# Optimization experiments

Measured on AMD Instinct MI355X. Metric: run time of the kernel, lower is better.

## Reference

```python
import jax, jax.numpy as jnp
from jax import lax
import numpy as np

DN = ('NHWC', 'HWIO', 'NHWC')  # NHWC activations, HWIO kernels (TF layout)
EPS = 1e-3


def setup_inputs() -> dict:
    key = jax.random.key(0)
    ks = jax.random.split(key, 6)
    B, H, W, C = 16, 64, 64, 256
    x = jax.random.normal(ks[0], (B, H, W, C), jnp.float32)
    # per-sample predicted kernels (scaled to keep activations well-conditioned)
    depthwise_kernels = jax.random.normal(ks[1], (B, 3, 3, C, C), jnp.float32) * 0.02
    pointwise_kernels = jax.random.normal(ks[2], (B, 1, 1, C, C), jnp.float32) * 0.06
    biases = jax.random.normal(ks[3], (B, C), jnp.float32) * 0.1
    # shared trailing Conv2D layer params
    conv_w = jax.random.normal(ks[4], (3, 3, C, C), jnp.float32) * 0.02
    conv_b = jnp.zeros((C,), jnp.float32)
    return dict(x=x, depthwise_kernels=depthwise_kernels,
                pointwise_kernels=pointwise_kernels, biases=biases,
                conv_w=conv_w, conv_b=conv_b)


def _instance_norm(x):
    # tf.nn.moments over spatial dims (population variance), eps=0.001
    mean = jnp.mean(x, axis=(1, 2), keepdims=True)
    var = jnp.var(x, axis=(1, 2), keepdims=True)
    return (x - mean) * lax.rsqrt(var + EPS)


def _reflect_pad_hw(x, p=1):
    pad = [(0, 0)] * (x.ndim - 3) + [(p, p), (p, p), (0, 0)]
    return jnp.pad(x, pad, mode='reflect')


def _per_sample_conv(xi, dk, pk, bi):
    # xi: [H,W,C]; dk: [3,3,C,Cm]; pk: [1,1,Cm,Co]; bi: [Co]
    xp = _reflect_pad_hw(xi)[None]  # [1,H+2,W+2,C]
    y = lax.conv_general_dilated(xp, dk, (1, 1), 'VALID', dimension_numbers=DN)
    y = lax.conv_general_dilated(y, pk, (1, 1), 'VALID', dimension_numbers=DN)
    return (y + bi)[0]


def reference(x, depthwise_kernels, pointwise_kernels, biases, conv_w, conv_b):
    x = _instance_norm(x)
    # per-sample kernels -> vmap over batch (replaces tf.map_fn)
    x = jax.vmap(_per_sample_conv)(x, depthwise_kernels, pointwise_kernels, biases)
    # shared Conv2D: reflect pad + VALID conv + bias
    xp = _reflect_pad_hw(x)
    y = lax.conv_general_dilated(xp, conv_w, (1, 1), 'VALID', dimension_numbers=DN)
    return y + conv_b
```

## Files before the change

kernel.cpp:

```cpp
#include <hip/hip_runtime.h>


typedef __bf16 bf16x8 __attribute__((ext_vector_type(8)));
typedef float f32x4 __attribute__((ext_vector_type(4)));

__device__ __forceinline__ float bf2f(unsigned short v) {
    return __uint_as_float(((unsigned int)v) << 16);
}
__device__ __forceinline__ unsigned short f2bf(float f) {
    unsigned int u = __float_as_uint(f);
    unsigned int r = (u + 0x7FFFu + ((u >> 16) & 1u)) >> 16;
    return (unsigned short)r;
}
__device__ __forceinline__ float ldg_elem(const void* p, size_t idx, bool isbf) {
    return isbf ? bf2f(((const unsigned short*)p)[idx]) : ((const float*)p)[idx];
}

__device__ __forceinline__ void gload16(const void* g, void* l) {
    __builtin_amdgcn_global_load_lds(
        (__attribute__((address_space(1))) void*)(unsigned long long)g,
        (__attribute__((address_space(3))) void*)(unsigned long long)l,
        16, 0, 0);
}

#define RAW_BARRIER() do { asm volatile("" ::: "memory"); \
                           __builtin_amdgcn_s_barrier();   \
                           asm volatile("" ::: "memory"); } while (0)

__global__ void detect_dtype(const unsigned short* __restrict__ x, int* __restrict__ flag) {
    __shared__ int wild;
    if (threadIdx.x == 0) wild = 0;
    __syncthreads();
    int cnt = 0;
    for (int i = 0; i < 16; ++i) {
        float a = fabsf(bf2f(x[threadIdx.x * 16 + i]));
        if (!(a < 64.f) || (a != 0.f && a < 1e-5f)) cnt++;
    }
    atomicAdd(&wild, cnt);
    __syncthreads();
    if (threadIdx.x == 0) *flag = (wild > 512) ? 0 : 1;
}

__global__ void norm_partial2(const void* __restrict__ x, const int* __restrict__ flag,
                              float* __restrict__ partS, float* __restrict__ partQ) {
    const bool isbf = (*flag != 0);
    const int b = blockIdx.x, ch = blockIdx.y;
    const int t = threadIdx.x;
    const int l = t & 63;
    const int c4 = l * 4;
    const int sp0 = t >> 6;
    const size_t base = ((size_t)(b * 4096 + ch * 128 + sp0)) * 256 + c4;
    float s[4] = {0.f, 0.f, 0.f, 0.f}, q[4] = {0.f, 0.f, 0.f, 0.f};
    if (isbf) {
        for (int i = 0; i < 32; ++i) {
            const unsigned short* p = (const unsigned short*)x + base + (size_t)i * 1024;
            ushort4 v = *(const ushort4*)p;
            float a[4] = {bf2f(v.x), bf2f(v.y), bf2f(v.z), bf2f(v.w)};
#pragma unroll
            for (int j = 0; j < 4; ++j) { s[j] += a[j]; q[j] += a[j] * a[j]; }
        }
    } else {
        for (int i = 0; i < 32; ++i) {
            float4 v = *(const float4*)((const float*)x + base + (size_t)i * 1024);
            float a[4] = {v.x, v.y, v.z, v.w};
#pragma unroll
            for (int j = 0; j < 4; ++j) { s[j] += a[j]; q[j] += a[j] * a[j]; }
        }
    }
    __shared__ float red[4][64][9];
#pragma unroll
    for (int j = 0; j < 4; ++j) { red[sp0][l][j] = s[j]; red[sp0][l][4 + j] = q[j]; }
    __syncthreads();
    if (t < 64) {
#pragma unroll
        for (int j = 0; j < 4; ++j) {
            float ss = red[0][t][j] + red[1][t][j] + red[2][t][j] + red[3][t][j];
            float qq = red[0][t][4 + j] + red[1][t][4 + j] + red[2][t][4 + j] + red[3][t][4 + j];
            int c = t * 4 + j;
            partS[(b * 32 + ch) * 256 + c] = ss;
            partQ[(b * 32 + ch) * 256 + c] = qq;
        }
    }
}

__global__ void norm_finalize2(const float* __restrict__ partS, const float* __restrict__ partQ,
                               float* __restrict__ mean, float* __restrict__ rstd) {
    const int b = blockIdx.x, c = threadIdx.x;
    float s = 0.f, q = 0.f;
    for (int k = 0; k < 32; ++k) {
        s += partS[(b * 32 + k) * 256 + c];
        q += partQ[(b * 32 + k) * 256 + c];
    }
    float m = s * (1.f / 4096.f);
    float v = q * (1.f / 4096.f) - m * m;
    mean[b * 256 + c] = m;
    rstd[b * 256 + c] = rsqrtf(v + 1e-3f);
}

__global__ void norm_apply(const void* __restrict__ x, const int* __restrict__ flag,
                           const float* __restrict__ mean, const float* __restrict__ rstd,
                           unsigned short* __restrict__ xn) {
    const bool isbf = (*flag != 0);
    size_t e = ((size_t)blockIdx.x * 256 + threadIdx.x) * 8;
    int c0 = (int)(e & 255);
    int bc = (int)(e >> 20) * 256 + c0;
    float v[8];
    if (isbf) {
        uint4 raw = *(const uint4*)((const unsigned short*)x + e);
        unsigned int rr[4] = {raw.x, raw.y, raw.z, raw.w};
#pragma unroll
        for (int i = 0; i < 4; ++i) {
            v[2 * i]     = bf2f((unsigned short)(rr[i] & 0xFFFF));
            v[2 * i + 1] = bf2f((unsigned short)(rr[i] >> 16));
        }
    } else {
        float4 f0 = *(const float4*)((const float*)x + e);
        float4 f1 = *(const float4*)((const float*)x + e + 4);
        v[0] = f0.x; v[1] = f0.y; v[2] = f0.z; v[3] = f0.w;
        v[4] = f1.x; v[5] = f1.y; v[6] = f1.z; v[7] = f1.w;
    }
    unsigned int o[4];
#pragma unroll
    for (int i = 0; i < 4; ++i) {
        unsigned short lo = f2bf((v[2 * i]     - mean[bc + 2 * i])     * rstd[bc + 2 * i]);
        unsigned short hi = f2bf((v[2 * i + 1] - mean[bc + 2 * i + 1]) * rstd[bc + 2 * i + 1]);
        o[i] = (unsigned int)lo | ((unsigned int)hi << 16);
    }
    uint4 out; out.x = o[0]; out.y = o[1]; out.z = o[2]; out.w = o[3];
    *(uint4*)(xn + e) = out;
}

template <bool SCALE>
__global__ void transpose_wk(const void* __restrict__ src, const int* __restrict__ flag,
                             unsigned short* __restrict__ dst,
                             int s_per, long dstBStride, int coStride,
                             const float* __restrict__ rstd) {
    __shared__ unsigned short tile[64][66];
    const bool isbf = (*flag != 0);
    const int sl = blockIdx.x;
    const int b = sl / s_per;
    const size_t dbase = (size_t)b * (size_t)dstBStride + (size_t)(sl % s_per) * 256;
    const int ci0 = blockIdx.y * 64, co0 = blockIdx.z * 64;
    const int t = threadIdx.x;
    const int co4 = (t & 15) * 4;
    const int r0 = t >> 4;
#pragma unroll
    for (int i = 0; i < 4; ++i) {
        int r = r0 + i * 16;
        size_t sidx = (size_t)sl * 65536 + (size_t)(ci0 + r) * 256 + co0 + co4;
        if (isbf) {
            ushort4 v = *(const ushort4*)((const unsigned short*)src + sidx);
            tile[r][co4] = v.x; tile[r][co4 + 1] = v.y;
            tile[r][co4 + 2] = v.z; tile[r][co4 + 3] = v.w;
        } else {
            float4 v = *(const float4*)((const float*)src + sidx);
            tile[r][co4] = f2bf(v.x); tile[r][co4 + 1] = f2bf(v.y);
            tile[r][co4 + 2] = f2bf(v.z); tile[r][co4 + 3] = f2bf(v.w);
        }
    }
    __syncthreads();
    const int cip = (t & 31) * 2;
    const int cob = t >> 5;
    float s0 = 1.f, s1 = 1.f;
    if (SCALE) { s0 = rstd[b * 256 + ci0 + cip]; s1 = rstd[b * 256 + ci0 + cip + 1]; }
#pragma unroll
    for (int i = 0; i < 8; ++i) {
        int co = cob + i * 8;
        unsigned short lo = tile[cip][co], hi = tile[cip + 1][co];
        if (SCALE) { lo = f2bf(bf2f(lo) * s0); hi = f2bf(bf2f(hi) * s1); }
        *(unsigned int*)(dst + dbase + (size_t)(co0 + co) * coStride + ci0 + cip) =
            (unsigned int)lo | ((unsigned int)hi << 16);
    }
}

__global__ void corr_kernel(const unsigned short* __restrict__ dkT,
                            const float* __restrict__ mean,
                            float* __restrict__ negcorr) {
    const int b = blockIdx.x;
    const int lane = threadIdx.x & 63;
    const int co = blockIdx.y * 4 + (threadIdx.x >> 6);
    const unsigned short* wp = dkT + (size_t)(b * 256 + co) * 2304;
    const float* mb = mean + b * 256;
    const int ci0 = (lane & 31) * 8;
    float4 ma = *(const float4*)(mb + ci0);
    float4 mc = *(const float4*)(mb + ci0 + 4);
    float mm[8] = {ma.x, ma.y, ma.z, ma.w, mc.x, mc.y, mc.z, mc.w};
    float sum = 0.f;
#pragma unroll
    for (int c = 0; c < 5; ++c) {
        int k = c * 512 + lane * 8;
        if (k < 2304) {
            uint4 w = *(const uint4*)(wp + k);
            unsigned int wsv[4] = {w.x, w.y, w.z, w.w};
#pragma unroll
            for (int j = 0; j < 4; ++j) {
                sum += bf2f((unsigned short)(wsv[j] & 0xFFFF)) * mm[2 * j];
                sum += bf2f((unsigned short)(wsv[j] >> 16)) * mm[2 * j + 1];
            }
        }
    }
#pragma unroll
    for (int off = 32; off > 0; off >>= 1) sum += __shfl_down(sum, off);
    if (lane == 0) negcorr[b * 256 + co] = -sum;
}

template <bool PER_SAMPLE_W, int BIAS_MODE, bool OUT_F32>
__global__ __launch_bounds__(512, 2) void conv3x3_256(const unsigned short* __restrict__ src,
                                                      const int* __restrict__ flag,
                                                      const unsigned short* __restrict__ wT,
                                                      const void* __restrict__ bias,
                                                      void* __restrict__ dst) {
    constexpr int KTOT = 2304;
    extern __shared__ unsigned short smem[];

    const int t = threadIdx.x;
    const int lane = t & 63;
    const int wave = t >> 6;
    const int wr = wave >> 1;
    const int wc = wave & 1;
    const int bid = blockIdx.x + 16 * blockIdx.z;
    const int b  = (bid & 7) + ((bid >> 3) & 1) * 8;
    const int mt = bid >> 4;
    const int m0 = mt * 256;
    const int R0 = mt * 4;
    const unsigned short* srcB = src + (size_t)b * (4096 * 256);
    const unsigned short* wB = wT + (PER_SAMPLE_W ? (size_t)b * 256 * KTOT : (size_t)0);
    const bool in_bf = (BIAS_MODE >= 2) ? (*flag != 0) : true;

    const int wx = t >> 3;
    const int wg = ((t & 7) ^ (wx & 7)) << 3;
    int wrow[6];
#pragma unroll
    for (int u = 0; u < 6; ++u) {
        int r = R0 - 1 + u;
        wrow[u] = (r < 0) ? 1 : (r > 63 ? 62 : r);
    }
    const unsigned short* winsrc[6];
#pragma unroll
    for (int u = 0; u < 6; ++u)
        winsrc[u] = srcB + ((size_t)wrow[u] * 64 + wx) * 256 + wg;
    const unsigned short* bsrc = wB + (size_t)wx * KTOT + wg;

    auto issueB = [&](int jn) {
        const int sn = jn % 9, cgn = jn / 9;
        const int koff = sn * 256 + cgn * 64;
        unsigned short* bdst = smem + 49152 + (jn & 1) * 16384 + wave * 512;
#pragma unroll
        for (int u = 0; u < 4; ++u)
            gload16(bsrc + (size_t)u * 64 * KTOT + koff, bdst + u * 4096);
    };

    f32x4 acc[4][8];
#pragma unroll
    for (int i = 0; i < 4; ++i)
#pragma unroll
        for (int j = 0; j < 8; ++j) acc[i][j] = (f32x4){0.f, 0.f, 0.f, 0.f};

    const int fr = lane & 15;
    const int quad = lane >> 4;
    const int fsw = fr & 7;
    const int ksb0 = (quad ^ fsw) << 3;
    const int ksb1 = ((quad + 4) ^ fsw) << 3;
    const int cn = wc * 128;

#pragma unroll
    for (int u = 0; u < 6; ++u)
        gload16(winsrc[u], smem + u * 4096 + wave * 512);
    issueB(0);

    bf16x8 afp[4][2], bfr[4][2];

    for (int cg = 0; cg < 4; ++cg) {
        const unsigned short* winb = smem + (cg & 1) * 24576;
        for (int s = 0; s < 9; ++s) {
            const int j = cg * 9 + s;
            const int dh = s / 3 - 1;
            const int dw = s % 3 - 1;

            const int keep = (cg < 3) ? ((s == 6 || s == 7) ? 2 : (s == 8 ? 1 : 0)) : 0;
            if (keep == 2)      asm volatile("s_waitcnt vmcnt(2)" ::: "memory");
            else if (keep == 1) asm volatile("s_waitcnt vmcnt(1)" ::: "memory");
            else                asm volatile("s_waitcnt vmcnt(0)" ::: "memory");
            RAW_BARRIER();

            if (j < 35) issueB(j + 1);
            if (cg < 3) {
                unsigned short* wdst = smem + ((cg + 1) & 1) * 24576 + wave * 512;
                const int cgo = (cg + 1) * 64;
                if (s == 5) {
                    gload16(winsrc[0] + cgo, wdst);
                    gload16(winsrc[1] + cgo, wdst + 4096);
                } else if (s == 6) {
                    gload16(winsrc[2] + cgo, wdst + 2 * 4096);
                    gload16(winsrc[3] + cgo, wdst + 3 * 4096);
                } else if (s == 7) {
                    gload16(winsrc[4] + cgo, wdst + 4 * 4096);
                } else if (s == 8) {
                    gload16(winsrc[5] + cgo, wdst + 5 * 4096);
                }
            }

            const unsigned short* Bb = smem + 49152 + (j & 1) * 16384;

#pragma unroll
            for (int n = 0; n < 4; ++n) {
                const unsigned short* rp = Bb + (cn + n * 16 + fr) * 64;
                bfr[n][0] = *(const bf16x8*)(rp + ksb0);
                bfr[n][1] = *(const bf16x8*)(rp + ksb1);
            }
            if (s == 0) {
                const unsigned short* A1 = winb + (wr + 1 + dh) * 4096;
#pragma unroll
                for (int mi = 0; mi < 4; ++mi) {
                    int ww = mi * 16 + fr + dw;
                    ww = (ww < 0) ? 1 : (ww > 63 ? 62 : ww);
                    const int x7 = ww & 7;
                    afp[mi][0] = *(const bf16x8*)(A1 + ww * 64 + ((quad ^ x7) << 3));
                    afp[mi][1] = *(const bf16x8*)(A1 + ww * 64 + (((quad + 4) ^ x7) << 3));
                }
            }

            __builtin_amdgcn_s_setprio(1);
#pragma unroll
            for (int mi = 0; mi < 4; ++mi)
#pragma unroll
                for (int n = 0; n < 4; ++n) {
                    acc[mi][n] = __builtin_amdgcn_mfma_f32_16x16x32_bf16(afp[mi][0], bfr[n][0], acc[mi][n], 0, 0, 0);
                    acc[mi][n] = __builtin_amdgcn_mfma_f32_16x16x32_bf16(afp[mi][1], bfr[n][1], acc[mi][n], 0, 0, 0);
                }
            __builtin_amdgcn_s_setprio(0);

#pragma unroll
            for (int n = 0; n < 4; ++n) {
                const unsigned short* rp = Bb + (cn + (n + 4) * 16 + fr) * 64;
                bfr[n][0] = *(const bf16x8*)(rp + ksb0);
                bfr[n][1] = *(const bf16x8*)(rp + ksb1);
            }

            __builtin_amdgcn_s_setprio(1);
#pragma unroll
            for (int mi = 0; mi < 4; ++mi)
#pragma unroll
                for (int n = 0; n < 4; ++n) {
                    acc[mi][n + 4] = __builtin_amdgcn_mfma_f32_16x16x32_bf16(afp[mi][0], bfr[n][0], acc[mi][n + 4], 0, 0, 0);
                    acc[mi][n + 4] = __builtin_amdgcn_mfma_f32_16x16x32_bf16(afp[mi][1], bfr[n][1], acc[mi][n + 4], 0, 0, 0);
                }
            __builtin_amdgcn_s_setprio(0);

            if (s < 8) {
                const int s1 = s + 1;
                const int dh1 = s1 / 3 - 1;
                const int dw1 = s1 % 3 - 1;
                const unsigned short* A1n = winb + (wr + 1 + dh1) * 4096;
#pragma unroll
                for (int mi = 0; mi < 4; ++mi) {
                    int ww = mi * 16 + fr + dw1;
                    ww = (ww < 0) ? 1 : (ww > 63 ? 62 : ww);
                    const int x7 = ww & 7;
                    afp[mi][0] = *(const bf16x8*)(A1n + ww * 64 + ((quad ^ x7) << 3));
                    afp[mi][1] = *(const bf16x8*)(A1n + ww * 64 + (((quad + 4) ^ x7) << 3));
                }
            }
        }
    }

    const int rbase = quad * 4;
    float bv[8];
#pragma unroll
    for (int n = 0; n < 8; ++n) {
        int nn = cn + n * 16 + fr;
        if (BIAS_MODE == 2)      bv[n] = ldg_elem(bias, b * 256 + nn, in_bf);
        else if (BIAS_MODE == 3) bv[n] = ldg_elem(bias, nn, in_bf);
        else                     bv[n] = 0.f;
    }
#pragma unroll
    for (int m = 0; m < 4; ++m) {
#pragma unroll
        for (int rr = 0; rr < 4; ++rr) {
            int mm = m0 + wr * 64 + m * 16 + rbase + rr;
            size_t rowoff = ((size_t)b * 4096 + mm) * 256;
#pragma unroll
            for (int n = 0; n < 8; ++n) {
                int nn = cn + n * 16 + fr;
                float val = acc[m][n][rr] + bv[n];
                if (OUT_F32) ((float*)dst)[rowoff + nn] = val;
                else         ((unsigned short*)dst)[rowoff + nn] = f2bf(val);
            }
        }
    }
}

template <int KSLICES, bool PER_SAMPLE_W, int BIAS_MODE, bool IS3X3, bool OUT_F32>
__global__ __launch_bounds__(512, 2) void gemm_conv_256(const unsigned short* __restrict__ src,
                                                        const int* __restrict__ flag,
                                                        const unsigned short* __restrict__ wT,
                                                        const void* __restrict__ bias,
                                                        void* __restrict__ dst) {
    constexpr int KTOT = KSLICES * 256;
    constexpr int NKT = KTOT / 64;
    static_assert(NKT >= 2, "pipeline needs >=2 K-tiles");
    extern __shared__ unsigned short smem[];

    const int t = threadIdx.x;
    const int lane = t & 63;
    const int wave = t >> 6;
    const int wr = wave >> 2;
    const int wc = wave & 3;
    const int bid = blockIdx.x + 16 * blockIdx.z;
    const int b  = (bid & 7) + ((bid >> 3) & 1) * 8;
    const int m0 = (bid >> 4) * 256;
    const unsigned short* srcB = src + (size_t)b * (4096 * 256);
    const unsigned short* wB = wT + (PER_SAMPLE_W ? (size_t)b * 256 * KTOT : (size_t)0);
    const bool in_bf = (BIAS_MODE >= 2) ? (*flag != 0) : true;

    const int trow = t >> 3;
    const int tswz = ((t & 7) ^ (trow & 7)) << 3;
    int hU[4], wU[4];
#pragma unroll
    for (int u = 0; u < 4; ++u) {
        int m = m0 + u * 64 + trow;
        hU[u] = m >> 6; wU[u] = m & 63;
    }
    const unsigned short* gBu[4];
#pragma unroll
    for (int u = 0; u < 4; ++u)
        gBu[u] = wB + (size_t)(u * 64 + trow) * KTOT + tswz;

    f32x4 acc[8][4];
#pragma unroll
    for (int i = 0; i < 8; ++i)
#pragma unroll
        for (int j = 0; j < 4; ++j) acc[i][j] = (f32x4){0.f, 0.f, 0.f, 0.f};

    const int fr = lane & 15;
    const int quad = lane >> 4;
    const int fsw = fr & 7;
    const int ks0 = ((quad) ^ fsw) << 3;
    const int ks1 = ((quad + 4) ^ fsw) << 3;
    const int rm = wr * 128;
    const int cn = wc * 64;

#pragma unroll
    for (int kt = 0; kt < 2; ++kt) {
        const int pdh = IS3X3 ? -1 : 0;
        const int pdw = IS3X3 ? -1 : 0;
        const int pchb = (kt & 3) << 6;
        unsigned short* ldsAW = smem + kt * 32768 + wave * 512;
#pragma unroll
        for (int u = 0; u < 4; ++u) {
            int hh = hU[u] + pdh; hh = (hh < 0) ? 1 : (hh > 63 ? 62 : hh);
            int ww = wU[u] + pdw; ww = (ww < 0) ? 1 : (ww > 63 ? 62 : ww);
            gload16(srcB + (size_t)((hh << 6) + ww) * 256 + pchb + tswz, ldsAW + u * 4096);
        }
#pragma unroll
        for (int u = 0; u < 4; ++u)
            gload16(gBu[u] + (size_t)kt * 64, ldsAW + 16384 + u * 4096);
    }
    asm volatile("s_waitcnt vmcnt(8)" ::: "memory");
    RAW_BARRIER();

    bf16x8 af[4][2], bfr[4][2];
    size_t aoff[4];
    int cur_s = -1;

    for (int i = 0; i < NKT; ++i) {
        const int buf = i & 1;
        const unsigned short* As_b = smem + buf * 32768;
        const unsigned short* Bs_b = As_b + 16384;
        unsigned short* ldsAW = smem + buf * 32768 + wave * 512;
        const int kt2 = i + 2;
        const bool st = (kt2 < NKT);

#pragma unroll
        for (int m = 0; m < 4; ++m) {
            const unsigned short* rp = As_b + (rm + m * 16 + fr) * 64;
            af[m][0] = *(const bf16x8*)(rp + ks0);
            af[m][1] = *(const bf16x8*)(rp + ks1);
        }
#pragma unroll
        for (int n = 0; n < 2; ++n) {
            const unsigned short* rp = Bs_b + (cn + n * 16 + fr) * 64;
            bfr[n][0] = *(const bf16x8*)(rp + ks0);
            bfr[n][1] = *(const bf16x8*)(rp + ks1);
        }
        __builtin_amdgcn_s_setprio(1);
#pragma unroll
        for (int m = 0; m < 4; ++m)
#pragma unroll
            for (int n = 0; n < 2; ++n) {
                acc[m][n] = __builtin_amdgcn_mfma_f32_16x16x32_bf16(af[m][0], bfr[n][0], acc[m][n], 0, 0, 0);
                acc[m][n] = __builtin_amdgcn_mfma_f32_16x16x32_bf16(af[m][1], bfr[n][1], acc[m][n], 0, 0, 0);
            }
        __builtin_amdgcn_s_setprio(0);

#pragma unroll
        for (int n = 2; n < 4; ++n) {
            const unsigned short* rp = Bs_b + (cn + n * 16 + fr) * 64;
            bfr[n][0] = *(const bf16x8*)(rp + ks0);
            bfr[n][1] = *(const bf16x8*)(rp + ks1);
        }
        __builtin_amdgcn_s_setprio(1);
#pragma unroll
        for (int m = 0; m < 4; ++m)
#pragma unroll
            for (int n = 2; n < 4; ++n) {
                acc[m][n] = __builtin_amdgcn_mfma_f32_16x16x32_bf16(af[m][0], bfr[n][0], acc[m][n], 0, 0, 0);
                acc[m][n] = __builtin_amdgcn_mfma_f32_16x16x32_bf16(af[m][1], bfr[n][1], acc[m][n], 0, 0, 0);
            }
        __builtin_amdgcn_s_setprio(0);

#pragma unroll
        for (int m = 0; m < 4; ++m) {
            const unsigned short* rp = As_b + (rm + 64 + m * 16 + fr) * 64;
            af[m][0] = *(const bf16x8*)(rp + ks0);
            af[m][1] = *(const bf16x8*)(rp + ks1);
        }
        __builtin_amdgcn_s_setprio(1);
#pragma unroll
        for (int m = 0; m < 4; ++m)
#pragma unroll
            for (int n = 0; n < 4; ++n) {
                acc[4 + m][n] = __builtin_amdgcn_mfma_f32_16x16x32_bf16(af[m][0], bfr[n][0], acc[4 + m][n], 0, 0, 0);
                acc[4 + m][n] = __builtin_amdgcn_mfma_f32_16x16x32_bf16(af[m][1], bfr[n][1], acc[4 + m][n], 0, 0, 0);
            }
        __builtin_amdgcn_s_setprio(0);

        RAW_BARRIER();
        if (st) {
            if (IS3X3) {
                const int s2 = kt2 >> 2;
                if (s2 != cur_s) {
                    cur_s = s2;
                    const int dh2 = s2 / 3 - 1, dw2 = s2 % 3 - 1;
#pragma unroll
                    for (int u = 0; u < 4; ++u) {
                        int hh = hU[u] + dh2; hh = (hh < 0) ? 1 : (hh > 63 ? 62 : hh);
                        int ww = wU[u] + dw2; ww = (ww < 0) ? 1 : (ww > 63 ? 62 : ww);
                        aoff[u] = (size_t)((hh << 6) + ww) * 256 + tswz;
                    }
                }
            } else if (cur_s < 0) {
                cur_s = 0;
#pragma unroll
                for (int u = 0; u < 4; ++u)
                    aoff[u] = (size_t)((hU[u] << 6) + wU[u]) * 256 + tswz;
            }
            const int chb2 = (kt2 & 3) << 6;
#pragma unroll
            for (int u = 0; u < 4; ++u)
                gload16(srcB + aoff[u] + chb2, ldsAW + u * 4096);
#pragma unroll
            for (int u = 0; u < 4; ++u)
                gload16(gBu[u] + (size_t)kt2 * 64, ldsAW + 16384 + u * 4096);
            asm volatile("s_waitcnt vmcnt(8)" ::: "memory");
        } else if (i + 1 < NKT) {
            asm volatile("s_waitcnt vmcnt(0)" ::: "memory");
        }
        RAW_BARRIER();
    }

    const int rbase = quad * 4;
    float bv[4];
#pragma unroll
    for (int n = 0; n < 4; ++n) {
        int nn = cn + n * 16 + fr;
        if (BIAS_MODE == 2)      bv[n] = ldg_elem(bias, b * 256 + nn, in_bf);
        else if (BIAS_MODE == 3) bv[n] = ldg_elem(bias, nn, in_bf);
        else                     bv[n] = 0.f;
    }
#pragma unroll
    for (int m = 0; m < 8; ++m) {
#pragma unroll
        for (int rr = 0; rr < 4; ++rr) {
            int mm = m0 + rm + m * 16 + rbase + rr;
            size_t rowoff = ((size_t)b * 4096 + mm) * 256;
#pragma unroll
            for (int n = 0; n < 4; ++n) {
                int nn = cn + n * 16 + fr;
                float val = acc[m][n][rr] + bv[n];
                if (OUT_F32) ((float*)dst)[rowoff + nn] = val;
                else         ((unsigned short*)dst)[rowoff + nn] = f2bf(val);
            }
        }
    }
}

template <int KSLICES, bool PER_SAMPLE_W, int BIAS_MODE, bool IS3X3, bool SRC_ADAPT, bool OUT_F32>
__global__ __launch_bounds__(256) void gemm_conv(const void* __restrict__ src,
                                                 const int* __restrict__ flag,
                                                 const unsigned short* __restrict__ wT,
                                                 const void* __restrict__ bias,
                                                 void* __restrict__ dst) {
    constexpr int KTOT = KSLICES * 256;
    __shared__ unsigned short As[128][40];
    __shared__ unsigned short Bs[128][40];

    const bool in_bf = (SRC_ADAPT || BIAS_MODE >= 2) ? (*flag != 0) : true;
    const int t = threadIdx.x;
    const int b = blockIdx.z;
    const int m0 = blockIdx.x * 128;
    const int n0 = blockIdx.y * 128;
    const size_t srcOfs = (size_t)b * (4096 * 256);
    const unsigned short* wB = wT + (PER_SAMPLE_W ? (size_t)b * 256 * KTOT : (size_t)0);

    f32x4 acc[4][4];
#pragma unroll
    for (int i = 0; i < 4; ++i)
#pragma unroll
        for (int j = 0; j < 4; ++j) acc[i][j] = (f32x4){0.f, 0.f, 0.f, 0.f};

    const int lane = t & 63;
    const int wave = t >> 6;
    const int rm = (wave >> 1) * 64;
    const int cn = (wave & 1) * 64;
    const int fr = lane & 15;
    const int kg = (lane >> 4) * 8;

    for (int kk = 0; kk < KTOT / 32; ++kk) {
        const int k0 = kk * 32;
        const int s = k0 >> 8;
        const int ci0 = k0 & 255;
        const int dh = IS3X3 ? (s / 3) - 1 : 0;
        const int dw = IS3X3 ? (s % 3) - 1 : 0;
        __syncthreads();
#pragma unroll
        for (int cc = 0; cc < 2; ++cc) {
            int ch = t + cc * 256;
            int r = ch >> 2;
            int ko = (ch & 3) << 3;
            int m = m0 + r;
            int h = m >> 6, w = m & 63;
            if (IS3X3) {
                h += dh; h = (h < 0) ? 1 : (h > 63 ? 62 : h);
                w += dw; w = (w < 0) ? 1 : (w > 63 ? 62 : w);
            }
            size_t eidx = srcOfs + (size_t)((h << 6) + w) * 256 + ci0 + ko;
            if (!SRC_ADAPT || in_bf) {
                uint4 v = *(const uint4*)((const unsigned short*)src + eidx);
                *(uint4*)&As[r][ko] = v;
            } else {
                const float* sf = (const float*)src + eidx;
                float4 f0 = *(const float4*)sf;
                float4 f1 = *(const float4*)(sf + 4);
                uint4 v;
                v.x = (unsigned int)f2bf(f0.x) | ((unsigned int)f2bf(f0.y) << 16);
                v.y = (unsigned int)f2bf(f0.z) | ((unsigned int)f2bf(f0.w) << 16);
                v.z = (unsigned int)f2bf(f1.x) | ((unsigned int)f2bf(f1.y) << 16);
                v.w = (unsigned int)f2bf(f1.z) | ((unsigned int)f2bf(f1.w) << 16);
                *(uint4*)&As[r][ko] = v;
            }
        }
#pragma unroll
        for (int cc = 0; cc < 2; ++cc) {
            int ch = t + cc * 256;
            int n = ch >> 2;
            int ko = (ch & 3) << 3;
            uint4 v = *(const uint4*)(wB + (size_t)(n0 + n) * KTOT + k0 + ko);
            *(uint4*)&Bs[n][ko] = v;
        }
        __syncthreads();

        bf16x8 af[4], bfr[4];
#pragma unroll
        for (int i = 0; i < 4; ++i) af[i] = *(const bf16x8*)&As[rm + i * 16 + fr][kg];
#pragma unroll
        for (int j = 0; j < 4; ++j) bfr[j] = *(const bf16x8*)&Bs[cn + j * 16 + fr][kg];
#pragma unroll
        for (int i = 0; i < 4; ++i)
#pragma unroll
            for (int j = 0; j < 4; ++j)
                acc[i][j] = __builtin_amdgcn_mfma_f32_16x16x32_bf16(af[i], bfr[j], acc[i][j], 0, 0, 0);
    }

    const int rbase = (lane >> 4) * 4;
    const int col = lane & 15;
    float bv[4];
#pragma unroll
    for (int j = 0; j < 4; ++j) {
        int n = n0 + cn + j * 16 + col;
        if (BIAS_MODE == 1)      bv[j] = ((const float*)bias)[b * 256 + n];
        else if (BIAS_MODE == 2) bv[j] = ldg_elem(bias, b * 256 + n, in_bf);
        else if (BIAS_MODE == 3) bv[j] = ldg_elem(bias, n, in_bf);
        else                     bv[j] = 0.f;
    }
#pragma unroll
    for (int i = 0; i < 4; ++i) {
#pragma unroll
        for (int rr = 0; rr < 4; ++rr) {
            int m = m0 + rm + i * 16 + rbase + rr;
            size_t rowoff = ((size_t)b * 4096 + m) * 256;
#pragma unroll
            for (int j = 0; j < 4; ++j) {
                int n = n0 + cn + j * 16 + col;
                float val = acc[i][j][rr] + bv[j];
                if (OUT_F32) ((float*)dst)[rowoff + n] = val;
                else         ((unsigned short*)dst)[rowoff + n] = f2bf(val);
            }
        }
    }
}

extern "C" void kernel_launch(void* const* d_in, const int* in_sizes, int n_in,
                              void* d_out, int out_size, void* d_ws, size_t ws_size,
                              hipStream_t stream) {
    const void* x    = d_in[0];
    const void* dk   = d_in[1];
    const void* pk   = d_in[2];
    const void* bias = d_in[3];
    const void* cw   = d_in[4];
    const void* cb   = d_in[5];

    const size_t NEED_SMALL = 36896768u;
    const size_t NEED_BIG   = 55771136u;
    if (ws_size < NEED_SMALL) return;
    const bool big = (ws_size >= NEED_BIG);

    char* ws = (char*)d_ws;
    int*   flagp   = (int*)ws;
    float* meanp   = (float*)(ws + 1024);
    float* rstdp   = (float*)(ws + 17408);
    float* negcorr = (float*)(ws + 33792);
    unsigned short* pkT = (unsigned short*)(ws + 65536);
    unsigned short* cwT = (unsigned short*)(ws + 2162688);
    unsigned short* dkT = (unsigned short*)(ws + 3342336);
    unsigned short* xn  = (unsigned short*)(ws + 22216704);
    float* partS = (float*)(ws + 22216704);
    float* partQ = (float*)(ws + 22216704 + 524288);
    unsigned short* y2  = big ? xn : dkT;
    unsigned short* y1  = (unsigned short*)d_out;

    hipFuncSetAttribute(reinterpret_cast<const void*>(conv3x3_256<true, 0, false>),
                        hipFuncAttributeMaxDynamicSharedMemorySize, 163840);
    hipFuncSetAttribute(reinterpret_cast<const void*>(conv3x3_256<false, 3, true>),
                        hipFuncAttributeMaxDynamicSharedMemorySize, 163840);
    hipFuncSetAttribute(reinterpret_cast<const void*>(gemm_conv_256<1, true, 2, false, false>),
                        hipFuncAttributeMaxDynamicSharedMemorySize, 131072);

    detect_dtype<<<1, 256, 0, stream>>>((const unsigned short*)x, flagp);
    norm_partial2<<<dim3(16, 32), 256, 0, stream>>>(x, flagp, partS, partQ);
    norm_finalize2<<<16, 256, 0, stream>>>(partS, partQ, meanp, rstdp);

    transpose_wk<false><<<dim3(16, 4, 4), 256, 0, stream>>>(pk, flagp, pkT, 1, 65536L, 256, nullptr);
    transpose_wk<false><<<dim3(9, 4, 4), 256, 0, stream>>>(cw, flagp, cwT, 9, 0L, 2304, nullptr);

    if (big) {
        transpose_wk<false><<<dim3(144, 4, 4), 256, 0, stream>>>(dk, flagp, dkT, 9, 589824L, 2304, nullptr);
        norm_apply<<<8192, 256, 0, stream>>>(x, flagp, meanp, rstdp, xn);
        conv3x3_256<true, 0, false><<<dim3(16, 1, 16), 512, 163840, stream>>>(xn, flagp, dkT, nullptr, y1);
    } else {
        transpose_wk<true><<<dim3(144, 4, 4), 256, 0, stream>>>(dk, flagp, dkT, 9, 589824L, 2304, rstdp);
        corr_kernel<<<dim3(16, 64), 256, 0, stream>>>(dkT, meanp, negcorr);
        gemm_conv<9, true, 1, true, true, false><<<dim3(32, 2, 16), 256, 0, stream>>>(x, flagp, dkT, negcorr, y1);
    }

    gemm_conv_256<1, true, 2, false, false><<<dim3(16, 1, 16), 512, 131072, stream>>>(y1, flagp, pkT, bias, y2);
    conv3x3_256<false, 3, true><<<dim3(16, 1, 16), 512, 163840, stream>>>(y2, flagp, cwT, cb, d_out);
}
```

Baseline: 335.0 us.

## Split conv3x3 K-steps into halves with triple-buffered weight tiles

```diff
diff --git a/kernel.cpp b/kernel.cpp
--- a/kernel.cpp
+++ b/kernel.cpp
@@ -239,15 +239,17 @@
 #pragma unroll
     for (int u = 0; u < 6; ++u)
         winsrc[u] = srcB + ((size_t)wrow[u] * 64 + wx) * 256 + wg;
-    const unsigned short* bsrc = wB + (size_t)wx * KTOT + wg;
+
+    const int btrow = t >> 2;
+    const int bg = ((t & 3) ^ (btrow & 3)) << 3;
+    const unsigned short* bsrc = wB + (size_t)btrow * KTOT + bg;
 
     auto issueB = [&](int jn) {
-        const int sn = jn % 9, cgn = jn / 9;
-        const int koff = sn * 256 + cgn * 64;
-        unsigned short* bdst = smem + 49152 + (jn & 1) * 16384 + wave * 512;
-#pragma unroll
-        for (int u = 0; u < 4; ++u)
-            gload16(bsrc + (size_t)u * 64 * KTOT + koff, bdst + u * 4096);
+        const int cgn = jn / 18, scn = jn % 18;
+        const int koff = (scn >> 1) * 256 + cgn * 64 + (scn & 1) * 32;
+        unsigned short* bdst = smem + 49152 + (jn % 3) * 8192 + wave * 512;
+        gload16(bsrc + koff, bdst);
+        gload16(bsrc + (size_t)128 * KTOT + koff, bdst + 4096);
     };
 
     f32x4 acc[4][8];
@@ -258,110 +260,77 @@
 
     const int fr = lane & 15;
     const int quad = lane >> 4;
-    const int fsw = fr & 7;
-    const int ksb0 = (quad ^ fsw) << 3;
-    const int ksb1 = ((quad + 4) ^ fsw) << 3;
     const int cn = wc * 128;
+    const int bxor = (quad ^ ((cn + fr) & 3)) << 3;
+    int boff[8];
+#pragma unroll
+    for (int n = 0; n < 8; ++n) boff[n] = (cn + n * 16 + fr) * 32 + bxor;
+
+    auto readB = [&](int jn, int n) -> bf16x8 {
+        const unsigned short* slotb = smem + 49152 + (jn % 3) * 8192;
+        return *(const bf16x8*)(slotb + boff[n]);
+    };
+    auto readA = [&](int jn, int mi) -> bf16x8 {
+        const int cgn = jn / 18, scn = jn % 18;
+        const int tap = scn >> 1, half = scn & 1;
+        const int dh = tap / 3 - 1, dw = tap % 3 - 1;
+        const unsigned short* A1 = smem + (cgn & 1) * 24576 + (wr + 1 + dh) * 4096;
+        int ww = mi * 16 + fr + dw;
+        ww = (ww < 0) ? 1 : (ww > 63 ? 62 : ww);
+        return *(const bf16x8*)(A1 + ww * 64 + (((half * 4 + quad) ^ (ww & 7)) << 3));
+    };
 
 #pragma unroll
     for (int u = 0; u < 6; ++u)
         gload16(winsrc[u], smem + u * 4096 + wave * 512);
     issueB(0);
-
-    bf16x8 afp[4][2], bfr[4][2];
-
-    for (int cg = 0; cg < 4; ++cg) {
-        const unsigned short* winb = smem + (cg & 1) * 24576;
-        for (int s = 0; s < 9; ++s) {
-            const int j = cg * 9 + s;
-            const int dh = s / 3 - 1;
-            const int dw = s % 3 - 1;
-
-            const int keep = (cg < 3) ? ((s == 6 || s == 7) ? 2 : (s == 8 ? 1 : 0)) : 0;
-            if (keep == 2)      asm volatile("s_waitcnt vmcnt(2)" ::: "memory");
-            else if (keep == 1) asm volatile("s_waitcnt vmcnt(1)" ::: "memory");
-            else                asm volatile("s_waitcnt vmcnt(0)" ::: "memory");
-            RAW_BARRIER();
-
-            if (j < 35) issueB(j + 1);
-            if (cg < 3) {
-                unsigned short* wdst = smem + ((cg + 1) & 1) * 24576 + wave * 512;
-                const int cgo = (cg + 1) * 64;
-                if (s == 5) {
-                    gload16(winsrc[0] + cgo, wdst);
-                    gload16(winsrc[1] + cgo, wdst + 4096);
-                } else if (s == 6) {
-                    gload16(winsrc[2] + cgo, wdst + 2 * 4096);
-                    gload16(winsrc[3] + cgo, wdst + 3 * 4096);
-                } else if (s == 7) {
-                    gload16(winsrc[4] + cgo, wdst + 4 * 4096);
-                } else if (s == 8) {
-                    gload16(winsrc[5] + cgo, wdst + 5 * 4096);
-                }
-            }
-
-            const unsigned short* Bb = smem + 49152 + (j & 1) * 16384;
-
-#pragma unroll
-            for (int n = 0; n < 4; ++n) {
-                const unsigned short* rp = Bb + (cn + n * 16 + fr) * 64;
-                bfr[n][0] = *(const bf16x8*)(rp + ksb0);
-                bfr[n][1] = *(const bf16x8*)(rp + ksb1);
-            }
-            if (s == 0) {
-                const unsigned short* A1 = winb + (wr + 1 + dh) * 4096;
-#pragma unroll
-                for (int mi = 0; mi < 4; ++mi) {
-                    int ww = mi * 16 + fr + dw;
-                    ww = (ww < 0) ? 1 : (ww > 63 ? 62 : ww);
-                    const int x7 = ww & 7;
-                    afp[mi][0] = *(const bf16x8*)(A1 + ww * 64 + ((quad ^ x7) << 3));
-                    afp[mi][1] = *(const bf16x8*)(A1 + ww * 64 + (((quad + 4) ^ x7) << 3));
-                }
-            }
-
-            __builtin_amdgcn_s_setprio(1);
+    issueB(1);
+    asm volatile("s_waitcnt vmcnt(0)" ::: "memory");
+    RAW_BARRIER();
+
+    bf16x8 afA[4], afB[4], bfr[8];
+#pragma unroll
+    for (int mi = 0; mi < 4; ++mi) afA[mi] = readA(0, mi);
+#pragma unroll
+    for (int n = 0; n < 8; ++n) bfr[n] = readB(0, n);
+
+    auto step = [&](int j, bf16x8 (&afc)[4], bf16x8 (&afn)[4]) {
+        const int jm = j - 1;
+        const bool keep1 = (jm >= 0) && ((jm % 18) >= 8) && ((jm % 18) <= 13) && (jm < 54);
+        if (keep1) asm volatile("s_waitcnt vmcnt(1)" ::: "memory");
+        else       asm volatile("s_waitcnt vmcnt(0)" ::: "memory");
+        RAW_BARRIER();
+
+        const int cgj = j / 18, scj = j % 18;
+        if (j + 2 < 72) issueB(j + 2);
+        if (cgj < 3 && scj >= 8 && scj <= 13) {
+            const int u = scj - 8;
+            gload16(winsrc[u] + (cgj + 1) * 64,
+                    smem + ((cgj + 1) & 1) * 24576 + u * 4096 + wave * 512);
+        }
+        if (scj == 0 && j > 0) {
+#pragma unroll
+            for (int mi = 0; mi < 4; ++mi) afc[mi] = readA(j, mi);
+        }
+        const bool rdnext = (j < 71);
+        __builtin_amdgcn_s_setprio(1);
+#pragma unroll
+        for (int n = 0; n < 8; ++n) {
 #pragma unroll
             for (int mi = 0; mi < 4; ++mi)
-#pragma unroll
-                for (int n = 0; n < 4; ++n) {
-                    acc[mi][n] = __builtin_amdgcn_mfma_f32_16x16x32_bf16(afp[mi][0], bfr[n][0], acc[mi][n], 0, 0, 0);
-                    acc[mi][n] = __builtin_amdgcn_mfma_f32_16x16x32_bf16(afp[mi][1], bfr[n][1], acc[mi][n], 0, 0, 0);
-                }
-            __builtin_amdgcn_s_setprio(0);
-
-#pragma unroll
-            for (int n = 0; n < 4; ++n) {
-                const unsigned short* rp = Bb + (cn + (n + 4) * 16 + fr) * 64;
-                bfr[n][0] = *(const bf16x8*)(rp + ksb0);
-                bfr[n][1] = *(const bf16x8*)(rp + ksb1);
-            }
-
-            __builtin_amdgcn_s_setprio(1);
-#pragma unroll
-            for (int mi = 0; mi < 4; ++mi)
-#pragma unroll
-                for (int n = 0; n < 4; ++n) {
-                    acc[mi][n + 4] = __builtin_amdgcn_mfma_f32_16x16x32_bf16(afp[mi][0], bfr[n][0], acc[mi][n + 4], 0, 0, 0);
-                    acc[mi][n + 4] = __builtin_amdgcn_mfma_f32_16x16x32_bf16(afp[mi][1], bfr[n][1], acc[mi][n + 4], 0, 0, 0);
-                }
-            __builtin_amdgcn_s_setprio(0);
-
-            if (s < 8) {
-                const int s1 = s + 1;
-                const int dh1 = s1 / 3 - 1;
-                const int dw1 = s1 % 3 - 1;
-                const unsigned short* A1n = winb + (wr + 1 + dh1) * 4096;
-#pragma unroll
-                for (int mi = 0; mi < 4; ++mi) {
-                    int ww = mi * 16 + fr + dw1;
-                    ww = (ww < 0) ? 1 : (ww > 63 ? 62 : ww);
-                    const int x7 = ww & 7;
-                    afp[mi][0] = *(const bf16x8*)(A1n + ww * 64 + ((quad ^ x7) << 3));
-                    afp[mi][1] = *(const bf16x8*)(A1n + ww * 64 + (((quad + 4) ^ x7) << 3));
-                }
-            }
-        }
+                acc[mi][n] = __builtin_amdgcn_mfma_f32_16x16x32_bf16(afc[mi], bfr[n], acc[mi][n], 0, 0, 0);
+            if (rdnext) bfr[n] = readB(j + 1, n);
+        }
+        __builtin_amdgcn_s_setprio(0);
+        if (rdnext && ((j + 1) % 18 != 0)) {
+#pragma unroll
+            for (int mi = 0; mi < 4; ++mi) afn[mi] = readA(j + 1, mi);
+        }
+    };
+
+    for (int jj = 0; jj < 72; jj += 2) {
+        step(jj, afA, afB);
+        step(jj + 1, afB, afA);
     }
 
     const int rbase = quad * 4;
@@ -730,9 +699,9 @@
     unsigned short* y1  = (unsigned short*)d_out;
 
     hipFuncSetAttribute(reinterpret_cast<const void*>(conv3x3_256<true, 0, false>),
-                        hipFuncAttributeMaxDynamicSharedMemorySize, 163840);
+                        hipFuncAttributeMaxDynamicSharedMemorySize, 147456);
     hipFuncSetAttribute(reinterpret_cast<const void*>(conv3x3_256<false, 3, true>),
-                        hipFuncAttributeMaxDynamicSharedMemorySize, 163840);
+                        hipFuncAttributeMaxDynamicSharedMemorySize, 147456);
     hipFuncSetAttribute(reinterpret_cast<const void*>(gemm_conv_256<1, true, 2, false, false>),
                         hipFuncAttributeMaxDynamicSharedMemorySize, 131072);
 
@@ -746,7 +715,7 @@
     if (big) {
         transpose_wk<false><<<dim3(144, 4, 4), 256, 0, stream>>>(dk, flagp, dkT, 9, 589824L, 2304, nullptr);
         norm_apply<<<8192, 256, 0, stream>>>(x, flagp, meanp, rstdp, xn);
-        conv3x3_256<true, 0, false><<<dim3(16, 1, 16), 512, 163840, stream>>>(xn, flagp, dkT, nullptr, y1);
+        conv3x3_256<true, 0, false><<<dim3(16, 1, 16), 512, 147456, stream>>>(xn, flagp, dkT, nullptr, y1);
     } else {
         transpose_wk<true><<<dim3(144, 4, 4), 256, 0, stream>>>(dk, flagp, dkT, 9, 589824L, 2304, rstdp);
         corr_kernel<<<dim3(16, 64), 256, 0, stream>>>(dkT, meanp, negcorr);
@@ -754,5 +723,5 @@
     }
 
     gemm_conv_256<1, true, 2, false, false><<<dim3(16, 1, 16), 512, 131072, stream>>>(y1, flagp, pkT, bias, y2);
-    conv3x3_256<false, 3, true><<<dim3(16, 1, 16), 512, 163840, stream>>>(y2, flagp, cwT, cb, d_out);
-}
+    conv3x3_256<false, 3, true><<<dim3(16, 1, 16), 512, 147456, stream>>>(y2, flagp, cwT, cb, d_out);
+}
```

New measurement: 351.9 us. 1.05x slower.
